# Kernel optimization log

Measured on AMD Instinct MI355X. Metric: run time of the kernel, lower is better.

Reference implementation:

```python
import jax, jax.numpy as jnp
import numpy as np


def setup_inputs() -> dict:
    key = jax.random.key(0)
    # frames: stack of 4 feature maps, each [B, C, H, W]
    frames = jax.random.normal(key, (4, 8, 64, 160, 160), dtype=jnp.float32)
    return {"frames": frames}


def reference(frames) -> jnp.ndarray:
    # frames: [4, B, C, H, W]
    B, C = frames.shape[1], frames.shape[2]
    # V = cat(x1..x4, dim=1) -> [B, 4C, H, W]
    V = jnp.concatenate([frames[i] for i in range(4)], axis=1)
    outs = []
    for i in range(4):
        # Qi = cat([xi]*4, dim=1) -> [B, 4C, H, W]
        Qi = jnp.tile(frames[i], (1, 4, 1, 1))
        # softmax over the 4C channel axis, then gate V
        s = jax.nn.softmax(Qi * V, axis=1) * V  # [B, 4C, H, W]
        # chunk into 4 blocks of C channels and sum -> [B, C, H, W]
        outs.append(s.reshape(B, 4, C, *s.shape[2:]).sum(axis=1))
    return jnp.concatenate(outs, axis=1)  # [B, 4C, H, W]
```

## Files before the change

kernel.cpp:

```cpp
#include <hip/hip_runtime.h>


#define HW 25600
#define NP 32
#define ROW 257
#define TILES_PER_B 800

__device__ __forceinline__ float wave_allsum(float x) {
  int v;
  v = __builtin_amdgcn_update_dpp(0, __float_as_int(x), 0xB1, 0xf, 0xf, true);
  x += __int_as_float(v);
  v = __builtin_amdgcn_update_dpp(0, __float_as_int(x), 0x4E, 0xf, 0xf, true);
  x += __int_as_float(v);
  v = __builtin_amdgcn_update_dpp(0, __float_as_int(x), 0x141, 0xf, 0xf, true);
  x += __int_as_float(v);
  v = __builtin_amdgcn_update_dpp(0, __float_as_int(x), 0x140, 0xf, 0xf, true);
  x += __int_as_float(v);
  v = __builtin_amdgcn_update_dpp(0, __float_as_int(x), 0x142, 0xa, 0xf, false);
  x += __int_as_float(v);
  v = __builtin_amdgcn_update_dpp(0, __float_as_int(x), 0x143, 0xc, 0xf, false);
  x += __int_as_float(v);
  return __int_as_float(__builtin_amdgcn_readlane(__float_as_int(x), 63));
}

__global__ __launch_bounds__(256, 4) void fused_frame_softmax(
    const float* __restrict__ in, float* __restrict__ out) {
  __shared__ float Xs[NP * ROW];

  const int b  = blockIdx.x / TILES_PER_B;
  const int p0 = (blockIdx.x % TILES_PER_B) * NP;
  const int t  = threadIdx.x;

  #pragma unroll
  for (int it = 0; it < 8; ++it) {
    const int q  = it * 256 + t;
    const int ch = q >> 3;
    const int pq = (q & 7) << 2;
    const int j  = ch >> 6;
    const int c  = ch & 63;
    const float4 v = *reinterpret_cast<const float4*>(
        in + ((j * 8 + b) * 64 + c) * HW + p0 + pq);
    Xs[(pq + 0) * ROW + ch] = v.x;
    Xs[(pq + 1) * ROW + ch] = v.y;
    Xs[(pq + 2) * ROW + ch] = v.z;
    Xs[(pq + 3) * ROW + ch] = v.w;
  }
  __syncthreads();

  const int lane  = t & 63;
  const int wbase = (t >> 6) * 8;
  #pragma unroll 2
  for (int pp = 0; pp < 8; ++pp) {
    float* row = Xs + (wbase + pp) * ROW;
    const float x0 = row[lane];
    const float x1 = row[lane + 64];
    const float x2 = row[lane + 128];
    const float x3 = row[lane + 192];

    const float E00 = __expf(x0 * x0);
    const float E01 = __expf(x0 * x1);
    const float E02 = __expf(x0 * x2);
    const float E03 = __expf(x0 * x3);
    const float E11 = __expf(x1 * x1);
    const float E12 = __expf(x1 * x2);
    const float E13 = __expf(x1 * x3);
    const float E22 = __expf(x2 * x2);
    const float E23 = __expf(x2 * x3);
    const float E33 = __expf(x3 * x3);

    const float z0 = wave_allsum(E00 + E01 + E02 + E03);
    const float z1 = wave_allsum(E01 + E11 + E12 + E13);
    const float z2 = wave_allsum(E02 + E12 + E22 + E23);
    const float z3 = wave_allsum(E03 + E13 + E23 + E33);

    const float r0 = __builtin_amdgcn_rcpf(z0);
    const float r1 = __builtin_amdgcn_rcpf(z1);
    const float r2 = __builtin_amdgcn_rcpf(z2);
    const float r3 = __builtin_amdgcn_rcpf(z3);

    row[lane]       = (E00 * x0 + E01 * x1 + E02 * x2 + E03 * x3) * r0;
    row[lane + 64]  = (E01 * x0 + E11 * x1 + E12 * x2 + E13 * x3) * r1;
    row[lane + 128] = (E02 * x0 + E12 * x1 + E22 * x2 + E23 * x3) * r2;
    row[lane + 192] = (E03 * x0 + E13 * x1 + E23 * x2 + E33 * x3) * r3;
  }
  __syncthreads();

  #pragma unroll
  for (int it = 0; it < 8; ++it) {
    const int q  = it * 256 + t;
    const int ch = q >> 3;
    const int pq = (q & 7) << 2;
    float4 v;
    v.x = Xs[(pq + 0) * ROW + ch];
    v.y = Xs[(pq + 1) * ROW + ch];
    v.z = Xs[(pq + 2) * ROW + ch];
    v.w = Xs[(pq + 3) * ROW + ch];
    *reinterpret_cast<float4*>(out + (b * 256 + ch) * HW + p0 + pq) = v;
  }
}

extern "C" void kernel_launch(void* const* d_in, const int* in_sizes, int n_in,
                              void* d_out, int out_size, void* d_ws, size_t ws_size,
                              hipStream_t stream) {
  const float* in = (const float*)d_in[0];
  float* out      = (float*)d_out;
  fused_frame_softmax<<<dim3(8 * TILES_PER_B), dim3(256), 0, stream>>>(in, out);
}
```

Baseline: 345.6 us.

## Persist blocks over four pixel tiles with register prefetch and nontemporal memory ops

Each block now handles four consecutive 32-pixel tiles instead of one, giving a grid of 1600 blocks. The next tile's global loads are issued into registers before the current tile is computed, then swapped into shared memory during the write-out loop. Loads and stores use nontemporal builtins to bypass cache retention on this streaming kernel. The aim is to hide load latency behind compute, at the cost of 32 extra registers per thread, fewer blocks, and an extra barrier per tile.

```diff
diff --git a/kernel.cpp b/kernel.cpp
--- a/kernel.cpp
+++ b/kernel.cpp
@@ -5,6 +5,10 @@
 #define NP 32
 #define ROW 257
 #define TILES_PER_B 800
+#define TPB 4
+#define BLOCKS_PER_B 200
+
+typedef float f32x4 __attribute__((ext_vector_type(4)));
 
 __device__ __forceinline__ float wave_allsum(float x) {
   int v;
@@ -27,75 +31,107 @@
     const float* __restrict__ in, float* __restrict__ out) {
   __shared__ float Xs[NP * ROW];
 
-  const int b  = blockIdx.x / TILES_PER_B;
-  const int p0 = (blockIdx.x % TILES_PER_B) * NP;
-  const int t  = threadIdx.x;
+  const int b     = blockIdx.x / BLOCKS_PER_B;
+  const int pbase = (blockIdx.x % BLOCKS_PER_B) * (TPB * NP);
+  const int t     = threadIdx.x;
+
+
+  f32x4 pf[8];
 
   #pragma unroll
   for (int it = 0; it < 8; ++it) {
     const int q  = it * 256 + t;
     const int ch = q >> 3;
     const int pq = (q & 7) << 2;
-    const int j  = ch >> 6;
-    const int c  = ch & 63;
-    const float4 v = *reinterpret_cast<const float4*>(
-        in + ((j * 8 + b) * 64 + c) * HW + p0 + pq);
-    Xs[(pq + 0) * ROW + ch] = v.x;
-    Xs[(pq + 1) * ROW + ch] = v.y;
-    Xs[(pq + 2) * ROW + ch] = v.z;
-    Xs[(pq + 3) * ROW + ch] = v.w;
+    const int off = ((ch >> 6) * 512 + b * 64 + (ch & 63)) * HW + pbase + pq;
+    pf[it] = __builtin_nontemporal_load(
+        reinterpret_cast<const f32x4*>(in + off));
+  }
+  #pragma unroll
+  for (int it = 0; it < 8; ++it) {
+    const int q  = it * 256 + t;
+    const int ch = q >> 3;
+    const int pq = (q & 7) << 2;
+    Xs[(pq + 0) * ROW + ch] = pf[it].x;
+    Xs[(pq + 1) * ROW + ch] = pf[it].y;
+    Xs[(pq + 2) * ROW + ch] = pf[it].z;
+    Xs[(pq + 3) * ROW + ch] = pf[it].w;
   }
   __syncthreads();
 
   const int lane  = t & 63;
   const int wbase = (t >> 6) * 8;
-  #pragma unroll 2
-  for (int pp = 0; pp < 8; ++pp) {
-    float* row = Xs + (wbase + pp) * ROW;
-    const float x0 = row[lane];
-    const float x1 = row[lane + 64];
-    const float x2 = row[lane + 128];
-    const float x3 = row[lane + 192];
 
-    const float E00 = __expf(x0 * x0);
-    const float E01 = __expf(x0 * x1);
-    const float E02 = __expf(x0 * x2);
-    const float E03 = __expf(x0 * x3);
-    const float E11 = __expf(x1 * x1);
-    const float E12 = __expf(x1 * x2);
-    const float E13 = __expf(x1 * x3);
-    const float E22 = __expf(x2 * x2);
-    const float E23 = __expf(x2 * x3);
-    const float E33 = __expf(x3 * x3);
+  for (int k = 0; k < TPB; ++k) {
+    if (k + 1 < TPB) {
+      #pragma unroll
+      for (int it = 0; it < 8; ++it) {
+        const int q  = it * 256 + t;
+        const int ch = q >> 3;
+        const int pq = (q & 7) << 2;
+        const int off =
+            ((ch >> 6) * 512 + b * 64 + (ch & 63)) * HW + pbase + (k + 1) * NP + pq;
+        pf[it] = __builtin_nontemporal_load(
+            reinterpret_cast<const f32x4*>(in + off));
+      }
+    }
 
-    const float z0 = wave_allsum(E00 + E01 + E02 + E03);
-    const float z1 = wave_allsum(E01 + E11 + E12 + E13);
-    const float z2 = wave_allsum(E02 + E12 + E22 + E23);
-    const float z3 = wave_allsum(E03 + E13 + E23 + E33);
+    #pragma unroll 2
+    for (int pp = 0; pp < 8; ++pp) {
+      float* row = Xs + (wbase + pp) * ROW;
+      const float x0 = row[lane];
+      const float x1 = row[lane + 64];
+      const float x2 = row[lane + 128];
+      const float x3 = row[lane + 192];
 
-    const float r0 = __builtin_amdgcn_rcpf(z0);
-    const float r1 = __builtin_amdgcn_rcpf(z1);
-    const float r2 = __builtin_amdgcn_rcpf(z2);
-    const float r3 = __builtin_amdgcn_rcpf(z3);
+      const float E00 = __expf(x0 * x0);
+      const float E01 = __expf(x0 * x1);
+      const float E02 = __expf(x0 * x2);
+      const float E03 = __expf(x0 * x3);
+      const float E11 = __expf(x1 * x1);
+      const float E12 = __expf(x1 * x2);
+      const float E13 = __expf(x1 * x3);
+      const float E22 = __expf(x2 * x2);
+      const float E23 = __expf(x2 * x3);
+      const float E33 = __expf(x3 * x3);
 
-    row[lane]       = (E00 * x0 + E01 * x1 + E02 * x2 + E03 * x3) * r0;
-    row[lane + 64]  = (E01 * x0 + E11 * x1 + E12 * x2 + E13 * x3) * r1;
-    row[lane + 128] = (E02 * x0 + E12 * x1 + E22 * x2 + E23 * x3) * r2;
-    row[lane + 192] = (E03 * x0 + E13 * x1 + E23 * x2 + E33 * x3) * r3;
-  }
-  __syncthreads();
+      const float z0 = wave_allsum(E00 + E01 + E02 + E03);
+      const float z1 = wave_allsum(E01 + E11 + E12 + E13);
+      const float z2 = wave_allsum(E02 + E12 + E22 + E23);
+      const float z3 = wave_allsum(E03 + E13 + E23 + E33);
 
-  #pragma unroll
-  for (int it = 0; it < 8; ++it) {
-    const int q  = it * 256 + t;
-    const int ch = q >> 3;
-    const int pq = (q & 7) << 2;
-    float4 v;
-    v.x = Xs[(pq + 0) * ROW + ch];
-    v.y = Xs[(pq + 1) * ROW + ch];
-    v.z = Xs[(pq + 2) * ROW + ch];
-    v.w = Xs[(pq + 3) * ROW + ch];
-    *reinterpret_cast<float4*>(out + (b * 256 + ch) * HW + p0 + pq) = v;
+      const float r0 = __builtin_amdgcn_rcpf(z0);
+      const float r1 = __builtin_amdgcn_rcpf(z1);
+      const float r2 = __builtin_amdgcn_rcpf(z2);
+      const float r3 = __builtin_amdgcn_rcpf(z3);
+
+      row[lane]       = (E00 * x0 + E01 * x1 + E02 * x2 + E03 * x3) * r0;
+      row[lane + 64]  = (E01 * x0 + E11 * x1 + E12 * x2 + E13 * x3) * r1;
+      row[lane + 128] = (E02 * x0 + E12 * x1 + E22 * x2 + E23 * x3) * r2;
+      row[lane + 192] = (E03 * x0 + E13 * x1 + E23 * x2 + E33 * x3) * r3;
+    }
+    __syncthreads();
+
+    #pragma unroll
+    for (int it = 0; it < 8; ++it) {
+      const int q  = it * 256 + t;
+      const int ch = q >> 3;
+      const int pq = (q & 7) << 2;
+      f32x4 v;
+      v.x = Xs[(pq + 0) * ROW + ch];
+      v.y = Xs[(pq + 1) * ROW + ch];
+      v.z = Xs[(pq + 2) * ROW + ch];
+      v.w = Xs[(pq + 3) * ROW + ch];
+      if (k + 1 < TPB) {
+        Xs[(pq + 0) * ROW + ch] = pf[it].x;
+        Xs[(pq + 1) * ROW + ch] = pf[it].y;
+        Xs[(pq + 2) * ROW + ch] = pf[it].z;
+        Xs[(pq + 3) * ROW + ch] = pf[it].w;
+      }
+      const int ooff = (b * 256 + ch) * HW + pbase + k * NP + pq;
+      __builtin_nontemporal_store(v, reinterpret_cast<f32x4*>(out + ooff));
+    }
+    __syncthreads();
   }
 }
 
@@ -104,5 +140,5 @@
                               hipStream_t stream) {
   const float* in = (const float*)d_in[0];
   float* out      = (float*)d_out;
-  fused_frame_softmax<<<dim3(8 * TILES_PER_B), dim3(256), 0, stream>>>(in, out);
+  fused_frame_softmax<<<dim3(8 * BLOCKS_PER_B), dim3(256), 0, stream>>>(in, out);
 }
```

New measurement: 344.3 us. No clear change (-0.4%).
